# Kernel tuning notes

Hardware: AMD Instinct MI355X
Metric: run time of the kernel (lower is better)

The kernel has to match this reference:

```python
import jax, jax.numpy as jnp
import numpy as np

N, E, P = 50000, 800000, 500000
NODE_IN, HIDDEN, EDGE_IN = 128, 256, 16


def setup_inputs() -> dict:
    key = jax.random.key(0)
    ks = jax.random.split(key, 16)
    s = lambda k, shape, fan_in: jax.random.normal(k, shape, jnp.float32) * (1.0 / np.sqrt(fan_in))
    return {
        "x": jax.random.normal(ks[0], (N, NODE_IN), jnp.float32),
        "edge_index": jax.random.randint(ks[1], (2, E), 0, N),
        "edge_u": jax.random.randint(ks[2], (P,), 0, N),
        "edge_v": jax.random.randint(ks[3], (P,), 0, N),
        "edge_attr": jax.random.normal(ks[4], (P, EDGE_IN), jnp.float32),
        "log_exposure": jax.random.normal(ks[5], (P,), jnp.float32),
        # conv1: lin_l (on mean-aggregated neighbors, with bias), lin_r (on root, no bias)
        "Wl1": s(ks[6], (HIDDEN, NODE_IN), NODE_IN),
        "bl1": jnp.zeros((HIDDEN,), jnp.float32),
        "Wr1": s(ks[7], (HIDDEN, NODE_IN), NODE_IN),
        # conv2
        "Wl2": s(ks[8], (HIDDEN, HIDDEN), HIDDEN),
        "bl2": jnp.zeros((HIDDEN,), jnp.float32),
        "Wr2": s(ks[9], (HIDDEN, HIDDEN), HIDDEN),
        # edge MLP: Linear(2*hidden+edge_in, hidden) -> ReLU -> Linear(hidden, 1)
        "W1": s(ks[10], (HIDDEN, 2 * HIDDEN + EDGE_IN), 2 * HIDDEN + EDGE_IN),
        "b1": jnp.zeros((HIDDEN,), jnp.float32),
        "W2": s(ks[11], (1, HIDDEN), HIDDEN),
        "b2": jnp.zeros((1,), jnp.float32),
    }


def sage_conv(x, src, dst, Wl, bl, Wr):
    # PyG SAGEConv, mean aggregation: out = lin_l(mean_{j in N(i)} x_j) + lin_r(x_i)
    n = x.shape[0]
    agg = jax.ops.segment_sum(x[src], dst, num_segments=n)          # [N, F]
    cnt = jax.ops.segment_sum(jnp.ones((src.shape[0],), x.dtype), dst, num_segments=n)
    agg = agg / jnp.maximum(cnt, 1.0)[:, None]
    return agg @ Wl.T + bl + x @ Wr.T


def reference(x, edge_index, edge_u, edge_v, edge_attr, log_exposure,
              Wl1, bl1, Wr1, Wl2, bl2, Wr2, W1, b1, W2, b2):
    src, dst = edge_index[0], edge_index[1]
    # eval mode: dropout is identity
    h = jax.nn.relu(sage_conv(x, src, dst, Wl1, bl1, Wr1))
    h = jax.nn.relu(sage_conv(h, src, dst, Wl2, bl2, Wr2))
    z = jnp.concatenate([h[edge_u], h[edge_v], edge_attr], axis=1)  # [P, 2H+Ein]
    s = (jax.nn.relu(z @ W1.T + b1) @ W2.T + b2)[:, 0]              # [P]
    return log_exposure + s
```

## Files before the change

kernel.cpp:

```cpp
#include <hip/hip_runtime.h>


typedef float f32x4 __attribute__((ext_vector_type(4)));
typedef float f32x2 __attribute__((ext_vector_type(2)));
typedef __bf16 bf16x8 __attribute__((ext_vector_type(8)));

__device__ __forceinline__ unsigned short f2b(float f) {
    unsigned u = __float_as_uint(f);
    u = u + 0x7fffu + ((u >> 16) & 1u);
    return (unsigned short)(u >> 16);
}
__device__ __forceinline__ float b2f(unsigned short s) {
    return __uint_as_float(((unsigned)s) << 16);
}
__device__ __forceinline__ float blo(unsigned x) { return b2f((unsigned short)(x & 0xffffu)); }
__device__ __forceinline__ float bhi(unsigned x) { return b2f((unsigned short)(x >> 16)); }
__device__ __forceinline__ int swz(int r, int g) { return (g + (r >> 1)) & 3; }
__device__ __forceinline__ unsigned char f2f8(float v) {
    return (unsigned char)(__builtin_amdgcn_cvt_pk_fp8_f32(v, v, 0, false) & 0xff);
}


__global__ void k_count(const int* __restrict__ dst, int* __restrict__ cnt, int E) {
    int e = blockIdx.x * 256 + threadIdx.x;
    if (e < E) atomicAdd(&cnt[dst[e]], 1);
}

__global__ __launch_bounds__(1024) void k_scan(int* __restrict__ cnt_cursor,
                                               int* __restrict__ row_ptr, int n) {
    __shared__ int wsum[16];
    __shared__ int carry;
    int t = threadIdx.x, lane = t & 63, w = t >> 6;
    if (t == 0) carry = 0;
    __syncthreads();
    int nch = (n + 1023) >> 10;
    for (int ch = 0; ch < nch; ++ch) {
        int i = (ch << 10) + t;
        int v = (i < n) ? cnt_cursor[i] : 0;
        int s = v;
        #pragma unroll
        for (int off = 1; off < 64; off <<= 1) {
            int u = __shfl_up(s, off);
            if (lane >= off) s += u;
        }
        if (lane == 63) wsum[w] = s;
        __syncthreads();
        int wpre = 0;
        for (int j = 0; j < w; ++j) wpre += wsum[j];
        int incl = s + wpre;
        int base = carry;
        if (i < n) { int ex = base + incl - v; row_ptr[i] = ex; cnt_cursor[i] = ex; }
        __syncthreads();
        if (t == 1023) carry = base + incl;
    }
    __syncthreads();
    if (t == 0) row_ptr[n] = carry;
}

__global__ void k_scatter(const int* __restrict__ src, const int* __restrict__ dst,
                          int* __restrict__ cursor, int* __restrict__ bucket, int E) {
    int e = blockIdx.x * 256 + threadIdx.x;
    if (e < E) {
        int p = atomicAdd(&cursor[dst[e]], 1);
        bucket[p] = src[e];
    }
}


__global__ void k_convert_weights(const float* __restrict__ Wl1, const float* __restrict__ Wr1,
                                  const float* __restrict__ Wl2, const float* __restrict__ Wr2,
                                  const float* __restrict__ W1, const float* __restrict__ b1,
                                  unsigned short* __restrict__ Wc1,
                                  unsigned short* __restrict__ Wc2,
                                  unsigned short* __restrict__ W1g,
                                  unsigned short* __restrict__ WaF) {
    int idx = blockIdx.x * 256 + threadIdx.x;
    if (idx < 65536) {
        int c = idx >> 13, j = (idx >> 5) & 255, kk = idx & 31;
        float v = (c < 4) ? Wl1[j * 128 + c * 32 + kk] : Wr1[j * 128 + (c - 4) * 32 + kk];
        Wc1[idx] = f2b(v);
    } else if (idx < 65536 + 131072) {
        int i2 = idx - 65536;
        int c = i2 >> 13, j = (i2 >> 5) & 255, kk = i2 & 31;
        float v = (c < 8) ? Wl2[j * 256 + c * 32 + kk] : Wr2[j * 256 + (c - 8) * 32 + kk];
        Wc2[i2] = f2b(v);
    } else if (idx < 65536 + 131072 + 131072) {
        int i3 = idx - 65536 - 131072;
        int c = i3 >> 14, j = (i3 >> 5) & 511, kk = i3 & 31;
        float v = (j < 256) ? W1[(size_t)j * 528 + c * 32 + kk]
                            : W1[(size_t)(j - 256) * 528 + 256 + c * 32 + kk];
        W1g[i3] = f2b(v);
    } else if (idx < 65536 + 131072 + 131072 + 8192) {
        int i4 = idx - 65536 - 131072 - 131072;
        int mi = i4 >> 9, l = (i4 >> 3) & 63, j = i4 & 7;
        int m = mi * 16 + (l & 15);
        int k = (l >> 4) * 8 + j;
        float v = (k < 16) ? W1[(size_t)m * 528 + 512 + k] : (k == 16 ? b1[m] : 0.f);
        WaF[i4] = f2b(v);
    }
}

__global__ void k_xconvert(const float* __restrict__ in, unsigned short* __restrict__ xb,
                           unsigned char* __restrict__ xf8, int n) {
    int j = (blockIdx.x * 256 + threadIdx.x) * 2;
    if (j < n) {
        float a = in[j], b = in[j + 1];
        xb[j] = f2b(a); xb[j + 1] = f2b(b);
        unsigned p = __builtin_amdgcn_cvt_pk_fp8_f32(a, b, 0, false);
        *reinterpret_cast<unsigned short*>(xf8 + j) = (unsigned short)(p & 0xffffu);
    }
}


__device__ __forceinline__ void accf8(uint2 v, float* s) {
    f32x2 p0 = __builtin_amdgcn_cvt_pk_f32_fp8(v.x, false);
    f32x2 p1 = __builtin_amdgcn_cvt_pk_f32_fp8(v.x, true);
    f32x2 p2 = __builtin_amdgcn_cvt_pk_f32_fp8(v.y, false);
    f32x2 p3 = __builtin_amdgcn_cvt_pk_f32_fp8(v.y, true);
    s[0] += p0.x; s[1] += p0.y; s[2] += p1.x; s[3] += p1.y;
    s[4] += p2.x; s[5] += p2.y; s[6] += p3.x; s[7] += p3.y;
}

__global__ __launch_bounds__(256) void k_agg_x(const unsigned char* __restrict__ xf8,
                                               const int* __restrict__ row_ptr,
                                               const int* __restrict__ bucket,
                                               unsigned short* __restrict__ agg, int Nn) {
    int node = blockIdx.x * 4 + (threadIdx.x >> 6);
    if (node >= Nn) return;
    int lane = threadIdx.x & 63;
    int q = lane >> 4, c = lane & 15;
    int beg = row_ptr[node], end = row_ptr[node + 1];
    int len = end - beg;
    int lo = beg + ((len * q) >> 2);
    int hi = beg + ((len * (q + 1)) >> 2);
    float s[8] = {0.f,0.f,0.f,0.f,0.f,0.f,0.f,0.f};
    const unsigned char* xp = xf8 + c * 8;
    int e = lo;
    for (; e + 4 <= hi; e += 4) {
        int b0 = bucket[e], b1 = bucket[e + 1], b2 = bucket[e + 2], b3 = bucket[e + 3];
        uint2 v0 = *reinterpret_cast<const uint2*>(xp + (size_t)b0 * 128);
        uint2 v1 = *reinterpret_cast<const uint2*>(xp + (size_t)b1 * 128);
        uint2 v2 = *reinterpret_cast<const uint2*>(xp + (size_t)b2 * 128);
        uint2 v3 = *reinterpret_cast<const uint2*>(xp + (size_t)b3 * 128);
        accf8(v0, s); accf8(v1, s); accf8(v2, s); accf8(v3, s);
    }
    for (; e < hi; ++e)
        accf8(*reinterpret_cast<const uint2*>(xp + (size_t)bucket[e] * 128), s);
    #pragma unroll
    for (int j = 0; j < 8; ++j) {
        s[j] += __shfl_xor(s[j], 16);
        s[j] += __shfl_xor(s[j], 32);
    }
    if (q == 0) {
        float sc = 1.0f / (float)(len > 1 ? len : 1);
        uint4 o;
        o.x = (unsigned)f2b(s[0]*sc) | ((unsigned)f2b(s[1]*sc) << 16);
        o.y = (unsigned)f2b(s[2]*sc) | ((unsigned)f2b(s[3]*sc) << 16);
        o.z = (unsigned)f2b(s[4]*sc) | ((unsigned)f2b(s[5]*sc) << 16);
        o.w = (unsigned)f2b(s[6]*sc) | ((unsigned)f2b(s[7]*sc) << 16);
        *reinterpret_cast<uint4*>(agg + (size_t)node * 128 + c * 8) = o;
    }
}

__global__ __launch_bounds__(256) void k_agg_h(const unsigned char* __restrict__ hf8,
                                               const int* __restrict__ row_ptr,
                                               const int* __restrict__ bucket,
                                               unsigned short* __restrict__ agg, int Nn) {
    int node = blockIdx.x * 4 + (threadIdx.x >> 6);
    if (node >= Nn) return;
    int lane = threadIdx.x & 63;
    int g = lane >> 5, c = lane & 31;
    int beg = row_ptr[node], end = row_ptr[node + 1];
    int len = end - beg;
    int lo = beg + ((len * g) >> 1);
    int hi = beg + ((len * (g + 1)) >> 1);
    float s[8] = {0.f,0.f,0.f,0.f,0.f,0.f,0.f,0.f};
    const unsigned char* hp = hf8 + c * 8;
    int e = lo;
    for (; e + 4 <= hi; e += 4) {
        int b0 = bucket[e], b1 = bucket[e + 1], b2 = bucket[e + 2], b3 = bucket[e + 3];
        uint2 v0 = *reinterpret_cast<const uint2*>(hp + (size_t)b0 * 256);
        uint2 v1 = *reinterpret_cast<const uint2*>(hp + (size_t)b1 * 256);
        uint2 v2 = *reinterpret_cast<const uint2*>(hp + (size_t)b2 * 256);
        uint2 v3 = *reinterpret_cast<const uint2*>(hp + (size_t)b3 * 256);
        accf8(v0, s); accf8(v1, s); accf8(v2, s); accf8(v3, s);
    }
    for (; e < hi; ++e)
        accf8(*reinterpret_cast<const uint2*>(hp + (size_t)bucket[e] * 256), s);
    #pragma unroll
    for (int j = 0; j < 8; ++j) s[j] += __shfl_xor(s[j], 32);
    if (g == 0) {
        float sc = 1.0f / (float)(len > 1 ? len : 1);
        uint4 o;
        o.x = (unsigned)f2b(s[0]*sc) | ((unsigned)f2b(s[1]*sc) << 16);
        o.y = (unsigned)f2b(s[2]*sc) | ((unsigned)f2b(s[3]*sc) << 16);
        o.z = (unsigned)f2b(s[4]*sc) | ((unsigned)f2b(s[5]*sc) << 16);
        o.w = (unsigned)f2b(s[6]*sc) | ((unsigned)f2b(s[7]*sc) << 16);
        *reinterpret_cast<uint4*>(agg + (size_t)node * 256 + c * 8) = o;
    }
}


__global__ __launch_bounds__(256) void k_conv_gemm(const unsigned short* __restrict__ Aagg,
                                                   const unsigned short* __restrict__ Aself,
                                                   const unsigned short* __restrict__ Wck,
                                                   const float* __restrict__ bias,
                                                   unsigned short* __restrict__ Hout,
                                                   unsigned char* __restrict__ Hf8,
                                                   int Nn, int F) {
    __shared__ __align__(16) unsigned short zt[128 * 32];
    __shared__ __align__(16) unsigned short wt[128 * 32];
    const int t = threadIdx.x;
    const int lane = t & 63, w = t >> 6;
    const int wm = w >> 1, wn = w & 1;
    const int node0 = blockIdx.x * 128;
    const int colh = blockIdx.y;
    const int half = F >> 5, nchunks = F >> 4;

    f32x4 acc[4][4];
    #pragma unroll
    for (int i = 0; i < 4; ++i)
        #pragma unroll
        for (int j = 0; j < 4; ++j) acc[i][j] = (f32x4){0.f, 0.f, 0.f, 0.f};

    for (int c = 0; c < nchunks; ++c) {
        __syncthreads();
        const unsigned short* Asrc = (c < half) ? Aagg : Aself;
        const int ccol = ((c < half) ? c : c - half) * 32;
        #pragma unroll
        for (int p = 0; p < 2; ++p) {
            int fc = t + p * 256;
            int row = fc >> 2, seg = fc & 3;
            int node = node0 + row; if (node >= Nn) node = Nn - 1;
            uint4 v = *reinterpret_cast<const uint4*>(Asrc + (size_t)node * F + ccol + seg * 8);
            *reinterpret_cast<uint4*>(&zt[row * 32 + swz(row, seg) * 8]) = v;
        }
        const unsigned short* Wsrc = Wck + ((size_t)c * 256 + colh * 128) * 32;
        #pragma unroll
        for (int p = 0; p < 2; ++p) {
            int fc = t + p * 256;
            int row = fc >> 2, seg = fc & 3;
            *reinterpret_cast<uint4*>(&wt[row * 32 + swz(row, seg) * 8]) =
                *reinterpret_cast<const uint4*>(Wsrc + fc * 8);
        }
        __syncthreads();
        bf16x8 a[4], b[4];
        const int q = lane >> 4;
        #pragma unroll
        for (int mi = 0; mi < 4; ++mi) {
            int R = wm * 64 + mi * 16 + (lane & 15);
            a[mi] = *reinterpret_cast<const bf16x8*>(&zt[R * 32 + swz(R, q) * 8]);
        }
        #pragma unroll
        for (int ni = 0; ni < 4; ++ni) {
            int R = wn * 64 + ni * 16 + (lane & 15);
            b[ni] = *reinterpret_cast<const bf16x8*>(&wt[R * 32 + swz(R, q) * 8]);
        }
        #pragma unroll
        for (int mi = 0; mi < 4; ++mi)
            #pragma unroll
            for (int ni = 0; ni < 4; ++ni)
                acc[mi][ni] = __builtin_amdgcn_mfma_f32_16x16x32_bf16(a[mi], b[ni], acc[mi][ni], 0, 0, 0);
    }

    #pragma unroll
    for (int mi = 0; mi < 4; ++mi)
        #pragma unroll
        for (int ni = 0; ni < 4; ++ni) {
            int col = colh * 128 + wn * 64 + ni * 16 + (lane & 15);
            float bia = bias[col];
            #pragma unroll
            for (int r = 0; r < 4; ++r) {
                int row = node0 + wm * 64 + mi * 16 + ((lane >> 4) << 2) + r;
                if (row < Nn) {
                    float v = acc[mi][ni][r] + bia;
                    v = v > 0.f ? v : 0.f;
                    Hout[(size_t)row * 256 + col] = f2b(v);
                    if (Hf8) Hf8[(size_t)row * 256 + col] = f2f8(v);
                }
            }
        }
}


__global__ __launch_bounds__(256) void k_gemm_g(const unsigned short* __restrict__ A,
                                                const unsigned short* __restrict__ Wck,
                                                unsigned short* __restrict__ Gout,
                                                int Nn) {
    __shared__ __align__(16) unsigned short zt[128 * 32];
    __shared__ __align__(16) unsigned short wt[128 * 32];
    const int t = threadIdx.x;
    const int lane = t & 63, w = t >> 6;
    const int wm = w >> 1, wn = w & 1;
    const int node0 = blockIdx.x * 128;
    const int colg = blockIdx.y;

    f32x4 acc[4][4];
    #pragma unroll
    for (int i = 0; i < 4; ++i)
        #pragma unroll
        for (int j = 0; j < 4; ++j) acc[i][j] = (f32x4){0.f, 0.f, 0.f, 0.f};

    for (int c = 0; c < 8; ++c) {
        __syncthreads();
        #pragma unroll
        for (int p = 0; p < 2; ++p) {
            int fc = t + p * 256;
            int row = fc >> 2, seg = fc & 3;
            int node = node0 + row; if (node >= Nn) node = Nn - 1;
            uint4 v = *reinterpret_cast<const uint4*>(A + (size_t)node * 256 + c * 32 + seg * 8);
            *reinterpret_cast<uint4*>(&zt[row * 32 + swz(row, seg) * 8]) = v;
        }
        const unsigned short* Wsrc = Wck + ((size_t)c * 512 + colg * 128) * 32;
        #pragma unroll
        for (int p = 0; p < 2; ++p) {
            int fc = t + p * 256;
            int row = fc >> 2, seg = fc & 3;
            *reinterpret_cast<uint4*>(&wt[row * 32 + swz(row, seg) * 8]) =
                *reinterpret_cast<const uint4*>(Wsrc + fc * 8);
        }
        __syncthreads();
        bf16x8 a[4], b[4];
        const int q = lane >> 4;
        #pragma unroll
        for (int mi = 0; mi < 4; ++mi) {
            int R = wm * 64 + mi * 16 + (lane & 15);
            a[mi] = *reinterpret_cast<const bf16x8*>(&zt[R * 32 + swz(R, q) * 8]);
        }
        #pragma unroll
        for (int ni = 0; ni < 4; ++ni) {
            int R = wn * 64 + ni * 16 + (lane & 15);
            b[ni] = *reinterpret_cast<const bf16x8*>(&wt[R * 32 + swz(R, q) * 8]);
        }
        #pragma unroll
        for (int mi = 0; mi < 4; ++mi)
            #pragma unroll
            for (int ni = 0; ni < 4; ++ni)
                acc[mi][ni] = __builtin_amdgcn_mfma_f32_16x16x32_bf16(a[mi], b[ni], acc[mi][ni], 0, 0, 0);
    }

    #pragma unroll
    for (int mi = 0; mi < 4; ++mi)
        #pragma unroll
        for (int ni = 0; ni < 4; ++ni) {
            int col = colg * 128 + wn * 64 + ni * 16 + (lane & 15);
            #pragma unroll
            for (int r = 0; r < 4; ++r) {
                int row = node0 + wm * 64 + mi * 16 + ((lane >> 4) << 2) + r;
                if (row < Nn)
                    Gout[(size_t)row * 512 + col] = f2b(acc[mi][ni][r]);
            }
        }
}


__global__ __launch_bounds__(256) void k_edge(const unsigned short* __restrict__ G2,
                                              const float* __restrict__ attr,
                                              const int* __restrict__ eu,
                                              const int* __restrict__ ev,
                                              const uint4* __restrict__ WaF,
                                              const float* __restrict__ W2,
                                              const float* __restrict__ b2,
                                              const float* __restrict__ logexp,
                                              float* __restrict__ out, int P) {
    __shared__ __align__(16) unsigned short attrT[64 * 40];
    __shared__ __align__(16) unsigned short guT[64 * 264];
    __shared__ __align__(16) unsigned short gvT[64 * 264];
    __shared__ float w2s[256];
    const int t = threadIdx.x;
    const int lane = t & 63, w = t >> 6;
    const int base = blockIdx.x * 64;

    {
        int e = t >> 2, seg = t & 3;
        int eg = base + e; if (eg >= P) eg = P - 1;
        const float4 f = *reinterpret_cast<const float4*>(attr + (size_t)eg * 16 + seg * 4);
        uint2 o;
        o.x = (unsigned)f2b(f.x) | ((unsigned)f2b(f.y) << 16);
        o.y = (unsigned)f2b(f.z) | ((unsigned)f2b(f.w) << 16);
        *reinterpret_cast<uint2*>(&attrT[e * 40 + seg * 4]) = o;
    }
    if (t < 64) {
        uint2 z0; z0.x = 0x3f80u; z0.y = 0u;
        *reinterpret_cast<uint2*>(&attrT[t * 40 + 16]) = z0;
        uint2 z1; z1.x = 0u; z1.y = 0u;
        *reinterpret_cast<uint2*>(&attrT[t * 40 + 20]) = z1;
        uint4 z2; z2.x = z2.y = z2.z = z2.w = 0u;
        *reinterpret_cast<uint4*>(&attrT[t * 40 + 24]) = z2;
    }
    w2s[t] = W2[t];
    __syncthreads();

    {
        const int h = lane >> 5, c = lane & 31;
        #pragma unroll
        for (int i = 0; i < 8; ++i) {
            int el = w * 16 + 2 * i + h;
            int eg = base + el; if (eg >= P) eg = P - 1;
            int u = eu[eg], v = ev[eg];
            uint4 a = *reinterpret_cast<const uint4*>(G2 + (size_t)u * 512 + c * 8);
            uint4 bb = *reinterpret_cast<const uint4*>(G2 + (size_t)v * 512 + 256 + c * 8);
            *reinterpret_cast<uint4*>(&guT[el * 264 + c * 8]) = a;
            *reinterpret_cast<uint4*>(&gvT[el * 264 + c * 8]) = bb;
        }
    }

    const int el = lane & 15, q = lane >> 4;
    const int grow = w * 16 + el;
    const bf16x8 bfrag = *reinterpret_cast<const bf16x8*>(&attrT[grow * 40 + q * 8]);
    float s = 0.f;
    #pragma unroll
    for (int mi = 0; mi < 16; ++mi) {
        const bf16x8 af = *reinterpret_cast<const bf16x8*>(&WaF[mi * 64 + lane]);
        f32x4 acc = __builtin_amdgcn_mfma_f32_16x16x32_bf16(af, bfrag, (f32x4){0.f,0.f,0.f,0.f}, 0, 0, 0);
        const uint2 gu2 = *reinterpret_cast<const uint2*>(&guT[grow * 264 + mi * 16 + q * 4]);
        const uint2 gv2 = *reinterpret_cast<const uint2*>(&gvT[grow * 264 + mi * 16 + q * 4]);
        const float4 w2v = *reinterpret_cast<const float4*>(&w2s[mi * 16 + q * 4]);
        float y0 = acc[0] + blo(gu2.x) + blo(gv2.x);
        float y1 = acc[1] + bhi(gu2.x) + bhi(gv2.x);
        float y2 = acc[2] + blo(gu2.y) + blo(gv2.y);
        float y3 = acc[3] + bhi(gu2.y) + bhi(gv2.y);
        s += (y0 > 0.f ? y0 : 0.f) * w2v.x;
        s += (y1 > 0.f ? y1 : 0.f) * w2v.y;
        s += (y2 > 0.f ? y2 : 0.f) * w2v.z;
        s += (y3 > 0.f ? y3 : 0.f) * w2v.w;
    }
    s += __shfl_xor(s, 16);
    s += __shfl_xor(s, 32);
    int eg = base + grow;
    if (q == 0 && eg < P)
        out[eg] = logexp[eg] + b2[0] + s;
}


extern "C" void kernel_launch(void* const* d_in, const int* in_sizes, int n_in,
                              void* d_out, int out_size, void* d_ws, size_t ws_size,
                              hipStream_t stream) {
    const float* x      = (const float*)d_in[0];
    const int*   eidx   = (const int*)d_in[1];
    const int*   eu     = (const int*)d_in[2];
    const int*   ev     = (const int*)d_in[3];
    const float* attr   = (const float*)d_in[4];
    const float* logexp = (const float*)d_in[5];
    const float* Wl1    = (const float*)d_in[6];
    const float* bl1    = (const float*)d_in[7];
    const float* Wr1    = (const float*)d_in[8];
    const float* Wl2    = (const float*)d_in[9];
    const float* bl2    = (const float*)d_in[10];
    const float* Wr2    = (const float*)d_in[11];
    const float* W1     = (const float*)d_in[12];
    const float* b1     = (const float*)d_in[13];
    const float* W2     = (const float*)d_in[14];
    const float* b2     = (const float*)d_in[15];
    float* out = (float*)d_out;

    const int N = in_sizes[0] / 128;
    const int E = in_sizes[1] / 2;
    const int P = in_sizes[2];
    const int* src = eidx;
    const int* dst = eidx + E;

    char* ws = (char*)d_ws;
    size_t off = 0;
    auto alloc = [&](size_t bytes) -> void* {
        off = (off + 255) & ~(size_t)255;
        void* p = ws + off;
        off += bytes;
        return p;
    };
    int* row_ptr = (int*)alloc((size_t)(N + 1) * 4);
    int* cursor  = (int*)alloc((size_t)N * 4);
    int* bucket  = (int*)alloc((size_t)E * 4);
    unsigned short* h1 = (unsigned short*)alloc((size_t)N * 256 * 2);
    unsigned short* h2 = (unsigned short*)alloc((size_t)N * 256 * 2);
    char* shared_base = (char*)alloc((size_t)N * 512 * 2);
    unsigned short* xb   = (unsigned short*)shared_base;
    unsigned short* agg1 = (unsigned short*)(shared_base + (size_t)N * 128 * 2);
    unsigned short* agg2 = (unsigned short*)(shared_base + (size_t)N * 256 * 2);
    unsigned short* G2   = (unsigned short*)shared_base;
    unsigned char* xf8  = (unsigned char*)alloc((size_t)N * 128);
    unsigned char* h1f8 = (unsigned char*)alloc((size_t)N * 256);
    unsigned short* Wc1  = (unsigned short*)alloc((size_t)65536 * 2);
    unsigned short* Wc2  = (unsigned short*)alloc((size_t)131072 * 2);
    unsigned short* W1g  = (unsigned short*)alloc((size_t)131072 * 2);
    unsigned short* WaF  = (unsigned short*)alloc((size_t)8192 * 2);

    hipMemsetAsync(cursor, 0, (size_t)N * 4, stream);
    k_count<<<(E + 255) / 256, 256, 0, stream>>>(dst, cursor, E);
    k_scan<<<1, 1024, 0, stream>>>(cursor, row_ptr, N);
    k_scatter<<<(E + 255) / 256, 256, 0, stream>>>(src, dst, cursor, bucket, E);
    k_convert_weights<<<(65536 + 131072 + 131072 + 8192 + 255) / 256, 256, 0, stream>>>(
        Wl1, Wr1, Wl2, Wr2, W1, b1, Wc1, Wc2, W1g, WaF);
    k_xconvert<<<(N * 64 + 255) / 256, 256, 0, stream>>>(x, xb, xf8, N * 128);

    k_agg_x<<<(N + 3) / 4, 256, 0, stream>>>(xf8, row_ptr, bucket, agg1, N);
    dim3 gconv((N + 127) / 128, 2);
    k_conv_gemm<<<gconv, 256, 0, stream>>>(agg1, xb, Wc1, bl1, h1, h1f8, N, 128);
    k_agg_h<<<(N + 3) / 4, 256, 0, stream>>>(h1f8, row_ptr, bucket, agg2, N);
    k_conv_gemm<<<gconv, 256, 0, stream>>>(agg2, h1, Wc2, bl2, h2, (unsigned char*)nullptr, N, 256);

    dim3 gg((N + 127) / 128, 4);
    k_gemm_g<<<gg, 256, 0, stream>>>(h2, W1g, G2, N);
    k_edge<<<(P + 63) / 64, 256, 0, stream>>>(G2, attr, eu, ev, (const uint4*)WaF,
                                              W2, b2, logexp, out, P);
}
```

Measured before the change: 534.5 us.

## Shrink edge-kernel LDS by pre-summing gathered rows in two column halves

```diff
diff --git a/kernel.cpp b/kernel.cpp
--- a/kernel.cpp
+++ b/kernel.cpp
@@ -15,6 +15,11 @@
 }
 __device__ __forceinline__ float blo(unsigned x) { return b2f((unsigned short)(x & 0xffffu)); }
 __device__ __forceinline__ float bhi(unsigned x) { return b2f((unsigned short)(x >> 16)); }
+__device__ __forceinline__ unsigned padd(unsigned a, unsigned b) {
+    float lo = __uint_as_float(a << 16) + __uint_as_float(b << 16);
+    float hi = __uint_as_float(a & 0xffff0000u) + __uint_as_float(b & 0xffff0000u);
+    return (__float_as_uint(hi) & 0xffff0000u) | (__float_as_uint(lo) >> 16);
+}
 __device__ __forceinline__ int swz(int r, int g) { return (g + (r >> 1)) & 3; }
 __device__ __forceinline__ unsigned char f2f8(float v) {
     return (unsigned char)(__builtin_amdgcn_cvt_pk_fp8_f32(v, v, 0, false) & 0xff);
@@ -354,19 +359,19 @@
 }
 
 
-__global__ __launch_bounds__(256) void k_edge(const unsigned short* __restrict__ G2,
-                                              const float* __restrict__ attr,
-                                              const int* __restrict__ eu,
-                                              const int* __restrict__ ev,
-                                              const uint4* __restrict__ WaF,
-                                              const float* __restrict__ W2,
-                                              const float* __restrict__ b2,
-                                              const float* __restrict__ logexp,
-                                              float* __restrict__ out, int P) {
+__global__ __launch_bounds__(256, 6) void k_edge(const unsigned short* __restrict__ G2,
+                                                 const float* __restrict__ attr,
+                                                 const int* __restrict__ eu,
+                                                 const int* __restrict__ ev,
+                                                 const uint4* __restrict__ WaF,
+                                                 const float* __restrict__ W2,
+                                                 const float* __restrict__ b2,
+                                                 const float* __restrict__ logexp,
+                                                 float* __restrict__ out, int P) {
     __shared__ __align__(16) unsigned short attrT[64 * 40];
-    __shared__ __align__(16) unsigned short guT[64 * 264];
-    __shared__ __align__(16) unsigned short gvT[64 * 264];
+    __shared__ __align__(16) unsigned short gt[64 * 132];
     __shared__ float w2s[256];
+    __shared__ int euv[128];
     const int t = threadIdx.x;
     const int lane = t & 63, w = t >> 6;
     const int base = blockIdx.x * 64;
@@ -388,42 +393,54 @@
         uint4 z2; z2.x = z2.y = z2.z = z2.w = 0u;
         *reinterpret_cast<uint4*>(&attrT[t * 40 + 24]) = z2;
     }
+    if (t < 128) {
+        int e = t >> 1;
+        int eg = base + e; if (eg >= P) eg = P - 1;
+        euv[t] = (t & 1) ? ev[eg] : eu[eg];
+    }
     w2s[t] = W2[t];
     __syncthreads();
-
-    {
-        const int h = lane >> 5, c = lane & 31;
-        #pragma unroll
-        for (int i = 0; i < 8; ++i) {
-            int el = w * 16 + 2 * i + h;
-            int eg = base + el; if (eg >= P) eg = P - 1;
-            int u = eu[eg], v = ev[eg];
-            uint4 a = *reinterpret_cast<const uint4*>(G2 + (size_t)u * 512 + c * 8);
-            uint4 bb = *reinterpret_cast<const uint4*>(G2 + (size_t)v * 512 + 256 + c * 8);
-            *reinterpret_cast<uint4*>(&guT[el * 264 + c * 8]) = a;
-            *reinterpret_cast<uint4*>(&gvT[el * 264 + c * 8]) = bb;
-        }
-    }
 
     const int el = lane & 15, q = lane >> 4;
     const int grow = w * 16 + el;
     const bf16x8 bfrag = *reinterpret_cast<const bf16x8*>(&attrT[grow * 40 + q * 8]);
+
     float s = 0.f;
     #pragma unroll
-    for (int mi = 0; mi < 16; ++mi) {
-        const bf16x8 af = *reinterpret_cast<const bf16x8*>(&WaF[mi * 64 + lane]);
-        f32x4 acc = __builtin_amdgcn_mfma_f32_16x16x32_bf16(af, bfrag, (f32x4){0.f,0.f,0.f,0.f}, 0, 0, 0);
-        const uint2 gu2 = *reinterpret_cast<const uint2*>(&guT[grow * 264 + mi * 16 + q * 4]);
-        const uint2 gv2 = *reinterpret_cast<const uint2*>(&gvT[grow * 264 + mi * 16 + q * 4]);
-        const float4 w2v = *reinterpret_cast<const float4*>(&w2s[mi * 16 + q * 4]);
-        float y0 = acc[0] + blo(gu2.x) + blo(gv2.x);
-        float y1 = acc[1] + bhi(gu2.x) + bhi(gv2.x);
-        float y2 = acc[2] + blo(gu2.y) + blo(gv2.y);
-        float y3 = acc[3] + bhi(gu2.y) + bhi(gv2.y);
-        s += (y0 > 0.f ? y0 : 0.f) * w2v.x;
-        s += (y1 > 0.f ? y1 : 0.f) * w2v.y;
-        s += (y2 > 0.f ? y2 : 0.f) * w2v.z;
-        s += (y3 > 0.f ? y3 : 0.f) * w2v.w;
+    for (int p = 0; p < 2; ++p) {
+        {
+            const int sub = lane >> 4, c = lane & 15;
+            #pragma unroll
+            for (int i = 0; i < 4; ++i) {
+                int le = w * 16 + i * 4 + sub;
+                int u = euv[2 * le], v = euv[2 * le + 1];
+                uint4 a = *reinterpret_cast<const uint4*>(G2 + (size_t)u * 512 + p * 128 + c * 8);
+                uint4 b = *reinterpret_cast<const uint4*>(G2 + (size_t)v * 512 + 256 + p * 128 + c * 8);
+                uint4 o;
+                o.x = padd(a.x, b.x);
+                o.y = padd(a.y, b.y);
+                o.z = padd(a.z, b.z);
+                o.w = padd(a.w, b.w);
+                *reinterpret_cast<uint4*>(&gt[le * 132 + c * 8]) = o;
+            }
+        }
+        #pragma unroll
+        for (int m = 0; m < 8; ++m) {
+            const int mi = p * 8 + m;
+            const bf16x8 af = *reinterpret_cast<const bf16x8*>(&WaF[mi * 64 + lane]);
+            f32x4 acc = __builtin_amdgcn_mfma_f32_16x16x32_bf16(af, bfrag, (f32x4){0.f,0.f,0.f,0.f}, 0, 0, 0);
+            const uint2 g2v = *reinterpret_cast<const uint2*>(&gt[grow * 132 + m * 16 + q * 4]);
+            const float4 w2v = *reinterpret_cast<const float4*>(&w2s[mi * 16 + q * 4]);
+            float y0 = acc[0] + blo(g2v.x);
+            float y1 = acc[1] + bhi(g2v.x);
+            float y2 = acc[2] + blo(g2v.y);
+            float y3 = acc[3] + bhi(g2v.y);
+            s += (y0 > 0.f ? y0 : 0.f) * w2v.x;
+            s += (y1 > 0.f ? y1 : 0.f) * w2v.y;
+            s += (y2 > 0.f ? y2 : 0.f) * w2v.z;
+            s += (y3 > 0.f ? y3 : 0.f) * w2v.w;
+        }
+        if (p == 0) __syncthreads();
     }
     s += __shfl_xor(s, 16);
     s += __shfl_xor(s, 32);
```

After: 503.4 us. 1.06x faster.
